# Optimization experiments

Hardware: AMD Instinct MI355X
Metric: run time of the kernel (lower is better)

The kernel has to match this reference:

```python
import jax, jax.numpy as jnp
import numpy as np

D_ENC, D_DEC, HID = 512, 512, 256

def setup_inputs() -> dict:
    key = jax.random.key(0)
    ks = jax.random.split(key, 8)
    B, T, U = 4, 800, 150
    enc = jax.random.normal(ks[0], (B, T, D_ENC), dtype=jnp.float32)
    dec = jax.random.normal(ks[1], (B, U, D_DEC), dtype=jnp.float32)
    s_e = 1.0 / np.sqrt(D_ENC)
    s_d = 1.0 / np.sqrt(D_DEC)
    s_h = 1.0 / np.sqrt(HID)
    W_enc = jax.random.uniform(ks[2], (D_ENC, HID), jnp.float32, -s_e, s_e)
    b_enc = jax.random.uniform(ks[3], (HID,), jnp.float32, -s_e, s_e)
    W_dec = jax.random.uniform(ks[4], (D_DEC, HID), jnp.float32, -s_d, s_d)
    b_dec = jax.random.uniform(ks[5], (HID,), jnp.float32, -s_d, s_d)
    w_score = jax.random.uniform(ks[6], (HID,), jnp.float32, -s_h, s_h)
    b_score = jax.random.uniform(ks[7], (), jnp.float32, -s_h, s_h)
    return {"encoder_out": enc, "decoder_out": dec,
            "W_enc": W_enc, "b_enc": b_enc,
            "W_dec": W_dec, "b_dec": b_dec,
            "w_score": w_score, "b_score": b_score}

def reference(encoder_out, decoder_out, W_enc, b_enc, W_dec, b_dec, w_score, b_score):
    # enc_proj: [B,T,H], dec_proj: [B,U,H]
    enc_proj = jnp.einsum('bte,eh->bth', encoder_out, W_enc) + b_enc
    dec_proj = jnp.einsum('bud,dh->buh', decoder_out, W_dec) + b_dec
    # Broadcast-add + tanh -> [B,T,U,H], then reduce H with score vector.
    combined = jnp.tanh(enc_proj[:, :, None, :] + dec_proj[:, None, :, :])
    score = jnp.einsum('btuh,h->btu', combined, w_score) + b_score
    # Softmax over decoder tokens (last dim U).
    return jax.nn.softmax(score, axis=-1)
```

## Files before the change

kernel.cpp:

```cpp
#include <hip/hip_runtime.h>
#include <hip/hip_bf16.h>

#define B_ 4
#define T_ 800
#define U_ 150
#define D_ 512
#define H_ 256
#define PADH2 132

static constexpr float ARG_SCALE = 2.8853900817779268f;
static constexpr float LOG2E_F   = 1.4426950408889634f;

typedef __attribute__((ext_vector_type(8))) short bf16x8;
typedef __attribute__((ext_vector_type(4))) float f32x4;

extern "C" __device__ float __ocml_exp2_f32(float);

__device__ __forceinline__ float fast_exp2(float x) {
#if __has_builtin(__builtin_amdgcn_exp2f)
    return __builtin_amdgcn_exp2f(x);
#else
    return __ocml_exp2_f32(x);
#endif
}
__device__ __forceinline__ float fast_rcp(float x) {
#if __has_builtin(__builtin_amdgcn_rcpf)
    return __builtin_amdgcn_rcpf(x);
#else
    return 1.0f / x;
#endif
}

__device__ __forceinline__ void bf16split(float x, unsigned short& hi, unsigned short& lo) {
    unsigned u = __builtin_bit_cast(unsigned, x);
    unsigned r = (u + 0x7FFFu + ((u >> 16) & 1u)) >> 16;
    hi = (unsigned short)r;
    float fh = __builtin_bit_cast(float, r << 16);
    float d = x - fh;
    unsigned u2 = __builtin_bit_cast(unsigned, d);
    unsigned r2 = (u2 + 0x7FFFu + ((u2 >> 16) & 1u)) >> 16;
    lo = (unsigned short)r2;
}

__global__ __launch_bounds__(256) void wconv_kernel(
    const float* __restrict__ We, const float* __restrict__ Wd,
    unsigned short* __restrict__ WtEh, unsigned short* __restrict__ WtEl,
    unsigned short* __restrict__ WtDh, unsigned short* __restrict__ WtDl)
{
    const int blk = blockIdx.x;
    const float* W; unsigned short *oh, *ol; int e;
    if (blk < 512) { W = We; oh = WtEh; ol = WtEl; e = blk; }
    else           { W = Wd; oh = WtDh; ol = WtDl; e = blk - 512; }
    const int h = threadIdx.x;
    float x = W[(size_t)e * H_ + h];
    unsigned short hi, lo; bf16split(x, hi, lo);
    const int s = e >> 5, q = (e >> 3) & 3, j = e & 7;
    const int g = h >> 4, r = h & 15, l = q * 16 + r;
    const size_t idx = (size_t)(s * 16 + g) * 512 + l * 8 + j;
    oh[idx] = hi; ol[idx] = lo;
}

__global__ __launch_bounds__(256) void proj_mfma_kernel(
    const float* __restrict__ enc, const float* __restrict__ dec,
    const unsigned short* __restrict__ WtEh, const unsigned short* __restrict__ WtEl,
    const unsigned short* __restrict__ WtDh, const unsigned short* __restrict__ WtDl,
    const float* __restrict__ b_enc, const float* __restrict__ b_dec,
    float* __restrict__ Ee, float* __restrict__ Ed)
{
    const int tid = threadIdx.x;
    int blk = blockIdx.x;
    const float* in; const unsigned short *Wh, *Wl; const float* bias; float* outp;
    int rmax;
    if (blk < 400) { in = enc; Wh = WtEh; Wl = WtEl; bias = b_enc; outp = Ee; rmax = B_ * T_ - 1; }
    else { blk -= 400; in = dec; Wh = WtDh; Wl = WtDl; bias = b_dec; outp = Ed; rmax = B_ * U_ - 1; }
    const int hh   = blk & 1;
    const int row0 = (blk >> 1) * 16;

    __shared__ unsigned short Ah[16 * 512];
    __shared__ unsigned short Al[16 * 512];

    #pragma unroll
    for (int k = 0; k < 4; ++k) {
        const int chunk = tid + 256 * k;
        const int r = chunk >> 6;
        const int c = chunk & 63;
        int gr = row0 + r; if (gr > rmax) gr = rmax;
        const float* src = in + (size_t)gr * D_ + c * 8;
        const float4 f0 = ((const float4*)src)[0];
        const float4 f1 = ((const float4*)src)[1];
        float v[8] = {f0.x, f0.y, f0.z, f0.w, f1.x, f1.y, f1.z, f1.w};
        bf16x8 ah, al;
        #pragma unroll
        for (int j = 0; j < 8; ++j) {
            unsigned short hi, lo; bf16split(v[j], hi, lo);
            ah[j] = (short)hi; al[j] = (short)lo;
        }
        const int di = r * 512 + ((c ^ (r & 7)) << 3);
        *(bf16x8*)&Ah[di] = ah;
        *(bf16x8*)&Al[di] = al;
    }
    __syncthreads();

    const int lane = tid & 63, w = tid >> 6;
    const int q = lane >> 4, r15 = lane & 15;

    f32x4 acc0 = {0.f, 0.f, 0.f, 0.f};
    f32x4 acc1 = {0.f, 0.f, 0.f, 0.f};

    const unsigned short* bh0 = Wh + (size_t)(8 * hh + 2 * w) * 512 + lane * 8;
    const unsigned short* bl0 = Wl + (size_t)(8 * hh + 2 * w) * 512 + lane * 8;

    #pragma unroll 4
    for (int s = 0; s < 16; ++s) {
        const int ai = r15 * 512 + ((((s << 2) + q) ^ (r15 & 7)) << 3);
        const bf16x8 ahf = *(const bf16x8*)&Ah[ai];
        const bf16x8 alf = *(const bf16x8*)&Al[ai];
        const size_t so = (size_t)(s * 16) * 512;
        const bf16x8 bh_0 = *(const bf16x8*)(bh0 + so);
        const bf16x8 bl_0 = *(const bf16x8*)(bl0 + so);
        const bf16x8 bh_1 = *(const bf16x8*)(bh0 + so + 512);
        const bf16x8 bl_1 = *(const bf16x8*)(bl0 + so + 512);
        acc0 = __builtin_amdgcn_mfma_f32_16x16x32_bf16(ahf, bh_0, acc0, 0, 0, 0);
        acc0 = __builtin_amdgcn_mfma_f32_16x16x32_bf16(ahf, bl_0, acc0, 0, 0, 0);
        acc0 = __builtin_amdgcn_mfma_f32_16x16x32_bf16(alf, bh_0, acc0, 0, 0, 0);
        acc1 = __builtin_amdgcn_mfma_f32_16x16x32_bf16(ahf, bh_1, acc1, 0, 0, 0);
        acc1 = __builtin_amdgcn_mfma_f32_16x16x32_bf16(ahf, bl_1, acc1, 0, 0, 0);
        acc1 = __builtin_amdgcn_mfma_f32_16x16x32_bf16(alf, bh_1, acc1, 0, 0, 0);
    }

    #pragma unroll
    for (int nt = 0; nt < 2; ++nt) {
        const int h = 128 * hh + 32 * w + nt * 16 + r15;
        const float bv = bias[h];
        const f32x4 a = nt ? acc1 : acc0;
        #pragma unroll
        for (int reg = 0; reg < 4; ++reg) {
            const int trow = row0 + 4 * q + reg;
            if (trow <= rmax)
                outp[(size_t)trow * H_ + h] = fast_exp2(ARG_SCALE * (a[reg] + bv));
        }
    }
}

__global__ __launch_bounds__(128) void score_kernel(
    const float* __restrict__ Ee, const float* __restrict__ Ed,
    const float* __restrict__ w_score,
    float* __restrict__ sc0, float* __restrict__ sc1)
{
    const int tid = threadIdx.x;
    const int ut = blockIdx.x % 5, hs = blockIdx.x / 5;
    const int tt = blockIdx.y, b = blockIdx.z;

    __shared__ float eld[32][PADH2];
    __shared__ float dld[32][PADH2];

    const int t0 = tt * 32, u0 = ut * 32;
    const int hoff = hs * 128;

    #pragma unroll
    for (int k = 0; k < 8; ++k) {
        int idx = tid + 128 * k;
        int row = idx >> 5;
        int f4  = idx & 31;
        *(float4*)&eld[row][4 * f4] =
            *(const float4*)(Ee + (size_t)(b * T_ + t0 + row) * H_ + hoff + 4 * f4);
        int du = u0 + row; if (du > U_ - 1) du = U_ - 1;
        *(float4*)&dld[row][4 * f4] =
            *(const float4*)(Ed + (size_t)(b * U_ + du) * H_ + hoff + 4 * f4);
    }
    __syncthreads();

    const int tx = tid & 15, ty = tid >> 4;
    const float* e0 = &eld[4 * ty + 0][0];
    const float* e1 = &eld[4 * ty + 1][0];
    const float* e2 = &eld[4 * ty + 2][0];
    const float* e3 = &eld[4 * ty + 3][0];
    const float* d0 = &dld[tx][0];
    const float* d1 = &dld[tx + 16][0];
    const float* wp = w_score + hoff;

    float4 z4 = {0.f, 0.f, 0.f, 0.f};
    float4 a00 = z4, a01 = z4, a10 = z4, a11 = z4;
    float4 a20 = z4, a21 = z4, a30 = z4, a31 = z4;

#define SIG(E, D) fast_rcp(fmaf((E), (D), 1.f))
#define ROW(A, EV, DV) \
    A.x = fmaf(w.x, SIG(EV.x, DV.x), A.x); \
    A.y = fmaf(w.y, SIG(EV.y, DV.y), A.y); \
    A.z = fmaf(w.z, SIG(EV.z, DV.z), A.z); \
    A.w = fmaf(w.w, SIG(EV.w, DV.w), A.w);

    #pragma unroll 4
    for (int h4 = 0; h4 < 32; ++h4) {
        float4 w  = ((const float4*)wp)[h4];
        float4 ea = *(const float4*)(e0 + 4 * h4);
        float4 eb = *(const float4*)(e1 + 4 * h4);
        float4 ec = *(const float4*)(e2 + 4 * h4);
        float4 ed = *(const float4*)(e3 + 4 * h4);
        float4 da = *(const float4*)(d0 + 4 * h4);
        float4 db = *(const float4*)(d1 + 4 * h4);
        ROW(a00, ea, da) ROW(a01, ea, db)
        ROW(a10, eb, da) ROW(a11, eb, db)
        ROW(a20, ec, da) ROW(a21, ec, db)
        ROW(a30, ed, da) ROW(a31, ed, db)
    }
#undef ROW
#undef SIG

    float s0[4], s1[4];
    s0[0] = (a00.x + a00.y) + (a00.z + a00.w);
    s0[1] = (a10.x + a10.y) + (a10.z + a10.w);
    s0[2] = (a20.x + a20.y) + (a20.z + a20.w);
    s0[3] = (a30.x + a30.y) + (a30.z + a30.w);
    s1[0] = (a01.x + a01.y) + (a01.z + a01.w);
    s1[1] = (a11.x + a11.y) + (a11.z + a11.w);
    s1[2] = (a21.x + a21.y) + (a21.z + a21.w);
    s1[3] = (a31.x + a31.y) + (a31.z + a31.w);

    float* sout = hs ? sc1 : sc0;
    const int ua = u0 + tx, ub = ua + 16;
    #pragma unroll
    for (int j = 0; j < 4; ++j) {
        const int t = t0 + 4 * ty + j;
        const size_t base = (size_t)(b * T_ + t) * U_;
        sout[base + ua] = s0[j];
        if (ub < U_) sout[base + ub] = s1[j];
    }
}

__global__ __launch_bounds__(256) void softmax_kernel(
    const float* __restrict__ sc0, const float* __restrict__ sc1,
    float* __restrict__ out)
{
    const int tid  = threadIdx.x;
    const int wave = tid >> 6, lane = tid & 63;
    const int row  = blockIdx.x * 4 + wave;
    const size_t base = (size_t)row * U_;

    float z0 = -2.f * (sc0[base + lane]      + sc1[base + lane]);
    float z1 = -2.f * (sc0[base + lane + 64] + sc1[base + lane + 64]);
    const bool v2 = (lane + 128) < U_;
    float z2 = v2 ? -2.f * (sc0[base + lane + 128] + sc1[base + lane + 128])
                  : -INFINITY;

    float m = fmaxf(fmaxf(z0, z1), z2);
    #pragma unroll
    for (int off = 32; off > 0; off >>= 1) m = fmaxf(m, __shfl_xor(m, off));

    float p0 = fast_exp2((z0 - m) * LOG2E_F);
    float p1 = fast_exp2((z1 - m) * LOG2E_F);
    float p2 = v2 ? fast_exp2((z2 - m) * LOG2E_F) : 0.f;

    float s = p0 + p1 + p2;
    #pragma unroll
    for (int off = 32; off > 0; off >>= 1) s += __shfl_xor(s, off);

    const float inv = 1.0f / s;
    out[base + lane]      = p0 * inv;
    out[base + lane + 64] = p1 * inv;
    if (v2) out[base + lane + 128] = p2 * inv;
}

extern "C" void kernel_launch(void* const* d_in, const int* in_sizes, int n_in,
                              void* d_out, int out_size, void* d_ws, size_t ws_size,
                              hipStream_t stream) {
    const float* enc     = (const float*)d_in[0];
    const float* dec     = (const float*)d_in[1];
    const float* W_enc   = (const float*)d_in[2];
    const float* b_enc   = (const float*)d_in[3];
    const float* W_dec   = (const float*)d_in[4];
    const float* b_dec   = (const float*)d_in[5];
    const float* w_score = (const float*)d_in[6];

    float* ws = (float*)d_ws;
    float* Ee  = ws;
    float* Ed  = Ee + 819200;
    float* sc0 = Ed + 153600;
    float* sc1 = sc0 + 480000;
    unsigned short* WtEh = (unsigned short*)(sc1 + 480000);
    unsigned short* WtEl = WtEh + 131072;
    unsigned short* WtDh = WtEl + 131072;
    unsigned short* WtDl = WtDh + 131072;
    float* out = (float*)d_out;

    wconv_kernel<<<1024, 256, 0, stream>>>(W_enc, W_dec, WtEh, WtEl, WtDh, WtDl);
    proj_mfma_kernel<<<476, 256, 0, stream>>>(enc, dec, WtEh, WtEl, WtDh, WtDl,
                                              b_enc, b_dec, Ee, Ed);
    score_kernel<<<dim3(10, 25, 4), 128, 0, stream>>>(Ee, Ed, w_score, sc0, sc1);
    softmax_kernel<<<800, 256, 0, stream>>>(sc0, sc1, out);
}
```

Measured before the change: 44.51 us.

## Batch four reciprocals into one and split projection across more blocks

The score loop now merges four terms of the form w/(1+e*d) into a single fraction, so it needs one reciprocal per four h values instead of four. Trading transcendental rcp calls for extra multiplies should relieve the special-function pipe. The projection kernel now computes one 16-column tile per wave, doubling the grid so more blocks are in flight, and ARG_SCALE is folded into the converted weights. Multiplying four denominators together risks overflow or precision loss when the exp-domain values are large.

Measured after the change: 41.51 us. -6.7%, faster.

```diff
diff --git a/kernel.cpp b/kernel.cpp
--- a/kernel.cpp
+++ b/kernel.cpp
@@ -52,7 +52,7 @@
     if (blk < 512) { W = We; oh = WtEh; ol = WtEl; e = blk; }
     else           { W = Wd; oh = WtDh; ol = WtDl; e = blk - 512; }
     const int h = threadIdx.x;
-    float x = W[(size_t)e * H_ + h];
+    float x = ARG_SCALE * W[(size_t)e * H_ + h];
     unsigned short hi, lo; bf16split(x, hi, lo);
     const int s = e >> 5, q = (e >> 3) & 3, j = e & 7;
     const int g = h >> 4, r = h & 15, l = q * 16 + r;
@@ -71,10 +71,10 @@
     int blk = blockIdx.x;
     const float* in; const unsigned short *Wh, *Wl; const float* bias; float* outp;
     int rmax;
-    if (blk < 400) { in = enc; Wh = WtEh; Wl = WtEl; bias = b_enc; outp = Ee; rmax = B_ * T_ - 1; }
-    else { blk -= 400; in = dec; Wh = WtDh; Wl = WtDl; bias = b_dec; outp = Ed; rmax = B_ * U_ - 1; }
-    const int hh   = blk & 1;
-    const int row0 = (blk >> 1) * 16;
+    if (blk < 800) { in = enc; Wh = WtEh; Wl = WtEl; bias = b_enc; outp = Ee; rmax = B_ * T_ - 1; }
+    else { blk -= 800; in = dec; Wh = WtDh; Wl = WtDl; bias = b_dec; outp = Ed; rmax = B_ * U_ - 1; }
+    const int hq   = blk & 3;
+    const int row0 = (blk >> 2) * 16;
 
     __shared__ unsigned short Ah[16 * 512];
     __shared__ unsigned short Al[16 * 512];
@@ -103,12 +103,11 @@
 
     const int lane = tid & 63, w = tid >> 6;
     const int q = lane >> 4, r15 = lane & 15;
-
-    f32x4 acc0 = {0.f, 0.f, 0.f, 0.f};
-    f32x4 acc1 = {0.f, 0.f, 0.f, 0.f};
-
-    const unsigned short* bh0 = Wh + (size_t)(8 * hh + 2 * w) * 512 + lane * 8;
-    const unsigned short* bl0 = Wl + (size_t)(8 * hh + 2 * w) * 512 + lane * 8;
+    const int g = 4 * hq + w;
+
+    f32x4 acc = {0.f, 0.f, 0.f, 0.f};
+    const unsigned short* bh0 = Wh + (size_t)g * 512 + lane * 8;
+    const unsigned short* bl0 = Wl + (size_t)g * 512 + lane * 8;
 
     #pragma unroll 4
     for (int s = 0; s < 16; ++s) {
@@ -116,29 +115,20 @@
         const bf16x8 ahf = *(const bf16x8*)&Ah[ai];
         const bf16x8 alf = *(const bf16x8*)&Al[ai];
         const size_t so = (size_t)(s * 16) * 512;
-        const bf16x8 bh_0 = *(const bf16x8*)(bh0 + so);
-        const bf16x8 bl_0 = *(const bf16x8*)(bl0 + so);
-        const bf16x8 bh_1 = *(const bf16x8*)(bh0 + so + 512);
-        const bf16x8 bl_1 = *(const bf16x8*)(bl0 + so + 512);
-        acc0 = __builtin_amdgcn_mfma_f32_16x16x32_bf16(ahf, bh_0, acc0, 0, 0, 0);
-        acc0 = __builtin_amdgcn_mfma_f32_16x16x32_bf16(ahf, bl_0, acc0, 0, 0, 0);
-        acc0 = __builtin_amdgcn_mfma_f32_16x16x32_bf16(alf, bh_0, acc0, 0, 0, 0);
-        acc1 = __builtin_amdgcn_mfma_f32_16x16x32_bf16(ahf, bh_1, acc1, 0, 0, 0);
-        acc1 = __builtin_amdgcn_mfma_f32_16x16x32_bf16(ahf, bl_1, acc1, 0, 0, 0);
-        acc1 = __builtin_amdgcn_mfma_f32_16x16x32_bf16(alf, bh_1, acc1, 0, 0, 0);
-    }
-
-    #pragma unroll
-    for (int nt = 0; nt < 2; ++nt) {
-        const int h = 128 * hh + 32 * w + nt * 16 + r15;
-        const float bv = bias[h];
-        const f32x4 a = nt ? acc1 : acc0;
-        #pragma unroll
-        for (int reg = 0; reg < 4; ++reg) {
-            const int trow = row0 + 4 * q + reg;
-            if (trow <= rmax)
-                outp[(size_t)trow * H_ + h] = fast_exp2(ARG_SCALE * (a[reg] + bv));
-        }
+        const bf16x8 bh = *(const bf16x8*)(bh0 + so);
+        const bf16x8 bl = *(const bf16x8*)(bl0 + so);
+        acc = __builtin_amdgcn_mfma_f32_16x16x32_bf16(ahf, bh, acc, 0, 0, 0);
+        acc = __builtin_amdgcn_mfma_f32_16x16x32_bf16(ahf, bl, acc, 0, 0, 0);
+        acc = __builtin_amdgcn_mfma_f32_16x16x32_bf16(alf, bh, acc, 0, 0, 0);
+    }
+
+    const int h = g * 16 + r15;
+    const float bv = bias[h];
+    #pragma unroll
+    for (int reg = 0; reg < 4; ++reg) {
+        const int trow = row0 + 4 * q + reg;
+        if (trow <= rmax)
+            outp[(size_t)trow * H_ + h] = fast_exp2(fmaf(ARG_SCALE, bv, acc[reg]));
     }
 }
 
@@ -179,16 +169,19 @@
     const float* d1 = &dld[tx + 16][0];
     const float* wp = w_score + hoff;
 
-    float4 z4 = {0.f, 0.f, 0.f, 0.f};
-    float4 a00 = z4, a01 = z4, a10 = z4, a11 = z4;
-    float4 a20 = z4, a21 = z4, a30 = z4, a31 = z4;
-
-#define SIG(E, D) fast_rcp(fmaf((E), (D), 1.f))
-#define ROW(A, EV, DV) \
-    A.x = fmaf(w.x, SIG(EV.x, DV.x), A.x); \
-    A.y = fmaf(w.y, SIG(EV.y, DV.y), A.y); \
-    A.z = fmaf(w.z, SIG(EV.z, DV.z), A.z); \
-    A.w = fmaf(w.w, SIG(EV.w, DV.w), A.w);
+    float a00 = 0.f, a01 = 0.f, a10 = 0.f, a11 = 0.f;
+    float a20 = 0.f, a21 = 0.f, a30 = 0.f, a31 = 0.f;
+
+#define QUAD(EV, DV, A) { \
+    float q0 = fmaf(EV.x, DV.x, 1.f); \
+    float q1 = fmaf(EV.y, DV.y, 1.f); \
+    float q2 = fmaf(EV.z, DV.z, 1.f); \
+    float q3 = fmaf(EV.w, DV.w, 1.f); \
+    float Dab = q0 * q1, Dcd = q2 * q3; \
+    float Nab = fmaf(w.x, q1, w.y * q0); \
+    float Ncd = fmaf(w.z, q3, w.w * q2); \
+    float N = fmaf(Nab, Dcd, Ncd * Dab); \
+    A = fmaf(N, fast_rcp(Dab * Dcd), A); }
 
     #pragma unroll 4
     for (int h4 = 0; h4 < 32; ++h4) {
@@ -199,23 +192,15 @@
         float4 ed = *(const float4*)(e3 + 4 * h4);
         float4 da = *(const float4*)(d0 + 4 * h4);
         float4 db = *(const float4*)(d1 + 4 * h4);
-        ROW(a00, ea, da) ROW(a01, ea, db)
-        ROW(a10, eb, da) ROW(a11, eb, db)
-        ROW(a20, ec, da) ROW(a21, ec, db)
-        ROW(a30, ed, da) ROW(a31, ed, db)
-    }
-#undef ROW
-#undef SIG
-
-    float s0[4], s1[4];
-    s0[0] = (a00.x + a00.y) + (a00.z + a00.w);
-    s0[1] = (a10.x + a10.y) + (a10.z + a10.w);
-    s0[2] = (a20.x + a20.y) + (a20.z + a20.w);
-    s0[3] = (a30.x + a30.y) + (a30.z + a30.w);
-    s1[0] = (a01.x + a01.y) + (a01.z + a01.w);
-    s1[1] = (a11.x + a11.y) + (a11.z + a11.w);
-    s1[2] = (a21.x + a21.y) + (a21.z + a21.w);
-    s1[3] = (a31.x + a31.y) + (a31.z + a31.w);
+        QUAD(ea, da, a00) QUAD(ea, db, a01)
+        QUAD(eb, da, a10) QUAD(eb, db, a11)
+        QUAD(ec, da, a20) QUAD(ec, db, a21)
+        QUAD(ed, da, a30) QUAD(ed, db, a31)
+    }
+#undef QUAD
+
+    float s0[4] = {a00, a10, a20, a30};
+    float s1[4] = {a01, a11, a21, a31};
 
     float* sout = hs ? sc1 : sc0;
     const int ua = u0 + tx, ub = ua + 16;
@@ -284,7 +269,7 @@
     float* out = (float*)d_out;
 
     wconv_kernel<<<1024, 256, 0, stream>>>(W_enc, W_dec, WtEh, WtEl, WtDh, WtDl);
-    proj_mfma_kernel<<<476, 256, 0, stream>>>(enc, dec, WtEh, WtEl, WtDh, WtDl,
+    proj_mfma_kernel<<<952, 256, 0, stream>>>(enc, dec, WtEh, WtEl, WtDh, WtDl,
                                               b_enc, b_dec, Ee, Ed);
     score_kernel<<<dim3(10, 25, 4), 128, 0, stream>>>(Ee, Ed, w_score, sc0, sc1);
     softmax_kernel<<<800, 256, 0, stream>>>(sc0, sc1, out);
```
